# Kernel tuning notes

Measured on AMD Instinct MI355X. Metric: run time of the kernel, lower is better.

Reference implementation:

```python
import jax, jax.numpy as jnp
import numpy as np

# Production-scale dims: N tokens = 64 batch x 8192 seq, hidden width 256.
N, D_IN, D_OUT = 524288, 256, 256
P_NONZERO = 0.05  # mimics bnn.random.calc_desired_var -> sparse ternary W


def binarise(v):
    # bnn.functions.binarise forward: sign with binarise(0) = +1
    return jnp.where(v >= 0, 1.0, -1.0).astype(v.dtype)


def setup_inputs() -> dict:
    key = jax.random.key(0)
    kx, kw = jax.random.split(key)
    # x: binary activations in {-1,+1} (output of a previous binarise layer)
    x = jnp.where(jax.random.normal(kx, (N, D_IN)) >= 0, 1.0, -1.0).astype(jnp.float32)
    # W: ternary {-1, 0, +1} with Var = P_NONZERO (values +-1 each w.p. p/2)
    u = jax.random.uniform(kw, (D_IN, D_OUT))
    W = jnp.where(u < P_NONZERO / 2, -1.0,
                  jnp.where(u < P_NONZERO, 1.0, 0.0)).astype(jnp.float32)
    return {"x": x, "W": W}


def reference(x, W):
    # integer = x @ W  (ternary-weight matmul; int math in torch, same values in fp32)
    integer = x @ W  # [N, D_OUT]
    return binarise(integer)
```

## Files before the change

kernel.cpp:

```cpp
#include <hip/hip_runtime.h>
#include <stdint.h>


#define NROWS  524288
#define DDIM   256
#define BLOCKS 2048
#define RPB    (NROWS / BLOCKS)
#define RPW    (RPB / 4)

typedef uint32_t u32;
typedef unsigned long long u64;

__global__ __launch_bounds__(256, 8)
void ternbin_kernel(const float* __restrict__ x, const float* __restrict__ W,
                    float* __restrict__ out) {
    __shared__ u32 signs[RPB][8];

    const int t    = threadIdx.x;
    const int lane = t & 63;
    const int wv   = t >> 6;
    const int col  = (wv << 6) | lane;

    u32 A0=0,A1=0,A2=0,A3=0,A4=0,A5=0,A6=0,A7=0;
    u32 M0=0,M1=0,M2=0,M3=0,M4=0,M5=0,M6=0,M7=0;
    #pragma unroll 8
    for (int k = 0; k < DDIM; ++k) {
        const float v = W[k * DDIM + col];
        const int   w = ((k & 3) << 1) | (k >> 7);
        const u32 bit = 1u << ((k >> 2) & 31);
        const u32 nz  = (v != 0.0f) ? bit : 0u;
        const u32 ng  = (v <  0.0f) ? bit : 0u;
        switch (w) {
            case 0: A0 |= nz; M0 |= ng; break;
            case 1: A1 |= nz; M1 |= ng; break;
            case 2: A2 |= nz; M2 |= ng; break;
            case 3: A3 |= nz; M3 |= ng; break;
            case 4: A4 |= nz; M4 |= ng; break;
            case 5: A5 |= nz; M5 |= ng; break;
            case 6: A6 |= nz; M6 |= ng; break;
            case 7: A7 |= nz; M7 |= ng; break;
        }
    }
    const int C = __popc(A0) + __popc(A1) + __popc(A2) + __popc(A3)
                + __popc(A4) + __popc(A5) + __popc(A6) + __popc(A7);

    const size_t row0 = (size_t)blockIdx.x * RPB;

    {
        const float* xp = x + (row0 + (size_t)wv * RPW) * DDIM + 4 * lane;
        const bool writer  = (lane < 8);
        const bool b2      = (lane & 4) != 0;
        const bool b1      = (lane & 2) != 0;
        const bool b0s     = (lane & 1) != 0;

        #pragma unroll 1
        for (int r = 0; r < RPW; r += 4) {
            uint4 v0 = *reinterpret_cast<const uint4*>(xp + (size_t)(r + 0) * DDIM);
            uint4 v1 = *reinterpret_cast<const uint4*>(xp + (size_t)(r + 1) * DDIM);
            uint4 v2 = *reinterpret_cast<const uint4*>(xp + (size_t)(r + 2) * DDIM);
            uint4 v3 = *reinterpret_cast<const uint4*>(xp + (size_t)(r + 3) * DDIM);

            #pragma unroll
            for (int i = 0; i < 4; ++i) {
                const uint4 v = (i == 0) ? v0 : (i == 1) ? v1 : (i == 2) ? v2 : v3;
                const u64 q0 = __ballot((int)v.x < 0);
                const u64 q1 = __ballot((int)v.y < 0);
                const u64 q2 = __ballot((int)v.z < 0);
                const u64 q3 = __ballot((int)v.w < 0);
                const u32 w0 = (u32)q0, w1 = (u32)(q0 >> 32);
                const u32 w2 = (u32)q1, w3 = (u32)(q1 >> 32);
                const u32 w4 = (u32)q2, w5 = (u32)(q2 >> 32);
                const u32 w6 = (u32)q3, w7 = (u32)(q3 >> 32);
                const u32 sel = b2 ? (b1 ? (b0s ? w7 : w6) : (b0s ? w5 : w4))
                                   : (b1 ? (b0s ? w3 : w2) : (b0s ? w1 : w0));
                if (writer) signs[wv * RPW + r + i][lane] = sel;
            }
        }
    }
    __syncthreads();

    float* oq = out + row0 * DDIM + col;
    #pragma unroll 2
    for (int r = 0; r < RPB; ++r) {
        const uint4 sa = *reinterpret_cast<const uint4*>(&signs[r][0]);
        const uint4 sb = *reinterpret_cast<const uint4*>(&signs[r][4]);
        int p = 0;
        p += __popc((sa.x ^ M0) & A0);
        p += __popc((sa.y ^ M1) & A1);
        p += __popc((sa.z ^ M2) & A2);
        p += __popc((sa.w ^ M3) & A3);
        p += __popc((sb.x ^ M4) & A4);
        p += __popc((sb.y ^ M5) & A5);
        p += __popc((sb.z ^ M6) & A6);
        p += __popc((sb.w ^ M7) & A7);
        const int d = C - 2 * p;
        const u32 o = 0x3f800000u | ((u32)d & 0x80000000u);
        __builtin_nontemporal_store(o,
            reinterpret_cast<u32*>(oq + (size_t)r * DDIM));
    }
}

extern "C" void kernel_launch(void* const* d_in, const int* in_sizes, int n_in,
                              void* d_out, int out_size, void* d_ws, size_t ws_size,
                              hipStream_t stream) {
    const float* x = (const float*)d_in[0];
    const float* W = (const float*)d_in[1];
    float* out = (float*)d_out;
    ternbin_kernel<<<BLOCKS, 256, 0, stream>>>(x, W, out);
}
```

Baseline: 982.9 us.

## Transpose output via lane shuffles to emit 16-byte nontemporal stores

Each thread now computes four consecutive rows for its column. A 4x4 transpose done with xor shuffles then lets each lane write four adjacent columns of one row as a single 128-bit nontemporal store, replacing four scalar 32-bit stores. This is meant to cut store instruction count and improve write coalescing on the output, which dominates traffic. It also adds a sched_barrier in the ballot stage and lowers the launch_bounds occupancy hint from 8 to 4, which adds shuffle and select overhead and may change register allocation.

```diff
diff --git a/kernel.cpp b/kernel.cpp
--- a/kernel.cpp
+++ b/kernel.cpp
@@ -10,8 +10,46 @@
 
 typedef uint32_t u32;
 typedef unsigned long long u64;
+typedef unsigned int u32x4 __attribute__((ext_vector_type(4)));
 
-__global__ __launch_bounds__(256, 8)
+#define BALLOT_STAGE(xv, ridx)                                            \
+    {                                                                     \
+        const u64 _q0 = __ballot((int)(xv).x < 0);                        \
+        const u64 _q1 = __ballot((int)(xv).y < 0);                        \
+        const u64 _q2 = __ballot((int)(xv).z < 0);                        \
+        const u64 _q3 = __ballot((int)(xv).w < 0);                        \
+        const u32 _w0 = (u32)_q0, _w1 = (u32)(_q0 >> 32);                 \
+        const u32 _w2 = (u32)_q1, _w3 = (u32)(_q1 >> 32);                 \
+        const u32 _w4 = (u32)_q2, _w5 = (u32)(_q2 >> 32);                 \
+        const u32 _w6 = (u32)_q3, _w7 = (u32)(_q3 >> 32);                 \
+        const u32 _sel = wb2 ? (wb1 ? (wb0 ? _w7 : _w6)                   \
+                                    : (wb0 ? _w5 : _w4))                  \
+                             : (wb1 ? (wb0 ? _w3 : _w2)                   \
+                                    : (wb0 ? _w1 : _w0));                 \
+        if (writer) signs[(ridx)][lane] = _sel;                           \
+    }
+
+#define DOTROW(dst, r)                                                    \
+    {                                                                     \
+        const uint4 _sa = *reinterpret_cast<const uint4*>(&signs[(r)][0]);\
+        const uint4 _sb = *reinterpret_cast<const uint4*>(&signs[(r)][4]);\
+        int _p = 0;                                                       \
+        _p += __popc((_sa.x ^ M0) & A0);                                  \
+        _p += __popc((_sa.y ^ M1) & A1);                                  \
+        _p += __popc((_sa.z ^ M2) & A2);                                  \
+        _p += __popc((_sa.w ^ M3) & A3);                                  \
+        _p += __popc((_sb.x ^ M4) & A4);                                  \
+        _p += __popc((_sb.y ^ M5) & A5);                                  \
+        _p += __popc((_sb.z ^ M6) & A6);                                  \
+        _p += __popc((_sb.w ^ M7) & A7);                                  \
+        const int _d = C - 2 * _p;                                        \
+        (dst) = 0x3f800000u | ((u32)_d & 0x80000000u);                    \
+    }
+
+#define PICK(j) (((j) & 2) ? (((j) & 1) ? o3 : o2) : (((j) & 1) ? o1 : o0))
+#define SEL(d) ((d) == 0 ? own : ((d) == 1 ? rr1 : ((d) == 2 ? rr2 : rr3)))
+
+__global__ __launch_bounds__(256, 4)
 void ternbin_kernel(const float* __restrict__ x, const float* __restrict__ W,
                     float* __restrict__ out) {
     __shared__ u32 signs[RPB][8];
@@ -48,10 +86,10 @@
 
     {
         const float* xp = x + (row0 + (size_t)wv * RPW) * DDIM + 4 * lane;
-        const bool writer  = (lane < 8);
-        const bool b2      = (lane & 4) != 0;
-        const bool b1      = (lane & 2) != 0;
-        const bool b0s     = (lane & 1) != 0;
+        const bool writer = (lane < 8);
+        const bool wb2 = (lane & 4) != 0;
+        const bool wb1 = (lane & 2) != 0;
+        const bool wb0 = (lane & 1) != 0;
 
         #pragma unroll 1
         for (int r = 0; r < RPW; r += 4) {
@@ -59,44 +97,40 @@
             uint4 v1 = *reinterpret_cast<const uint4*>(xp + (size_t)(r + 1) * DDIM);
             uint4 v2 = *reinterpret_cast<const uint4*>(xp + (size_t)(r + 2) * DDIM);
             uint4 v3 = *reinterpret_cast<const uint4*>(xp + (size_t)(r + 3) * DDIM);
-
-            #pragma unroll
-            for (int i = 0; i < 4; ++i) {
-                const uint4 v = (i == 0) ? v0 : (i == 1) ? v1 : (i == 2) ? v2 : v3;
-                const u64 q0 = __ballot((int)v.x < 0);
-                const u64 q1 = __ballot((int)v.y < 0);
-                const u64 q2 = __ballot((int)v.z < 0);
-                const u64 q3 = __ballot((int)v.w < 0);
-                const u32 w0 = (u32)q0, w1 = (u32)(q0 >> 32);
-                const u32 w2 = (u32)q1, w3 = (u32)(q1 >> 32);
-                const u32 w4 = (u32)q2, w5 = (u32)(q2 >> 32);
-                const u32 w6 = (u32)q3, w7 = (u32)(q3 >> 32);
-                const u32 sel = b2 ? (b1 ? (b0s ? w7 : w6) : (b0s ? w5 : w4))
-                                   : (b1 ? (b0s ? w3 : w2) : (b0s ? w1 : w0));
-                if (writer) signs[wv * RPW + r + i][lane] = sel;
-            }
+            __builtin_amdgcn_sched_barrier(0);
+            const int rb = wv * RPW + r;
+            BALLOT_STAGE(v0, rb + 0);
+            BALLOT_STAGE(v1, rb + 1);
+            BALLOT_STAGE(v2, rb + 2);
+            BALLOT_STAGE(v3, rb + 3);
         }
     }
     __syncthreads();
 
-    float* oq = out + row0 * DDIM + col;
+    const int s  = lane & 3;
+    const int q4 = lane & ~3;
+    float* oq = out + row0 * DDIM + (wv << 6) + q4;
+
     #pragma unroll 2
-    for (int r = 0; r < RPB; ++r) {
-        const uint4 sa = *reinterpret_cast<const uint4*>(&signs[r][0]);
-        const uint4 sb = *reinterpret_cast<const uint4*>(&signs[r][4]);
-        int p = 0;
-        p += __popc((sa.x ^ M0) & A0);
-        p += __popc((sa.y ^ M1) & A1);
-        p += __popc((sa.z ^ M2) & A2);
-        p += __popc((sa.w ^ M3) & A3);
-        p += __popc((sb.x ^ M4) & A4);
-        p += __popc((sb.y ^ M5) & A5);
-        p += __popc((sb.z ^ M6) & A6);
-        p += __popc((sb.w ^ M7) & A7);
-        const int d = C - 2 * p;
-        const u32 o = 0x3f800000u | ((u32)d & 0x80000000u);
-        __builtin_nontemporal_store(o,
-            reinterpret_cast<u32*>(oq + (size_t)r * DDIM));
+    for (int rp = 0; rp < RPB; rp += 4) {
+        u32 o0, o1, o2, o3;
+        DOTROW(o0, rp + 0);
+        DOTROW(o1, rp + 1);
+        DOTROW(o2, rp + 2);
+        DOTROW(o3, rp + 3);
+
+        const u32 own = PICK(s);
+        const u32 rr1 = __shfl_xor(PICK(s ^ 1), 1);
+        const u32 rr2 = __shfl_xor(PICK(s ^ 2), 2);
+        const u32 rr3 = __shfl_xor(PICK(s ^ 3), 3);
+        u32x4 ov;
+        ov.x = SEL(s);
+        ov.y = SEL(s ^ 1);
+        ov.z = SEL(s ^ 2);
+        ov.w = SEL(s ^ 3);
+
+        __builtin_nontemporal_store(ov,
+            reinterpret_cast<u32x4*>(oq + (size_t)(rp + s) * DDIM));
     }
 }
 
```

Measured after the change: 994.6 us. About the same (+1.2%).
